# Optimization experiments

Measured on AMD Instinct MI355X. Metric: run time of the kernel, lower is better.

Reference implementation:

```python
import jax, jax.numpy as jnp
import numpy as np

N_NODES = 50000
N_EDGES = 800000
D = 128  # hidden_dim == node feature dim


def setup_inputs() -> dict:
    key = jax.random.key(0)
    k1, k2, k3, k4 = jax.random.split(key, 4)
    node_feat = jax.random.normal(k1, (N_NODES, D), dtype=jnp.float32)
    edge_index = jax.random.randint(k2, (2, N_EDGES), 0, N_NODES, dtype=jnp.int32)
    # MLP params: LazyLinear(2D -> D), Linear(D -> D)
    W1 = jax.random.normal(k3, (2 * D, D), dtype=jnp.float32) * (1.0 / np.sqrt(2 * D))
    b1 = jnp.zeros((D,), dtype=jnp.float32)
    W2 = jax.random.normal(k4, (D, D), dtype=jnp.float32) * (1.0 / np.sqrt(D))
    b2 = jnp.zeros((D,), dtype=jnp.float32)
    return {"node_feat": node_feat, "edge_index": edge_index,
            "W1": W1, "b1": b1, "W2": W2, "b2": b2}


def reference(node_feat, edge_index, W1, b1, W2, b2):
    # node_feat: [N, D]; edge_index: [2, E]
    src, dst = edge_index[0], edge_index[1]
    n = node_feat.shape[0]
    # gather source feats [E, D], scatter-add into dst -> [N, D]
    msgs = node_feat[src]
    agg = jax.ops.segment_sum(msgs, dst, num_segments=n)
    # degree normalization (clamp min 1)
    deg = jax.ops.segment_sum(jnp.ones_like(dst, dtype=node_feat.dtype), dst,
                              num_segments=n)
    agg = agg / jnp.maximum(deg, 1.0)[:, None]
    # update MLP on concat([node_feat, agg]); dropout is identity at eval
    h = jnp.concatenate([node_feat, agg], axis=-1)          # [N, 2D]
    h = jax.nn.relu(h @ W1 + b1)                             # [N, D]
    h = jax.nn.relu(h @ W2 + b2)                             # [N, D]
    return h
```

## Files before the change

kernel.cpp:

```cpp
#include <hip/hip_runtime.h>
#include <hip/hip_bf16.h>

#define N_NODES 50000
#define N_EDGES 800000
#define D 128
#define SLOTS 64
#define NTILES 782

typedef __attribute__((ext_vector_type(8))) short short8v;
typedef __attribute__((ext_vector_type(4))) float f32x4;


__device__ __forceinline__ unsigned short f32_to_bf16_rn(float f) {
    unsigned int u = __float_as_uint(f);
    unsigned int r = (u + 0x7fffu + ((u >> 16) & 1u)) >> 16;
    return (unsigned short)r;
}
__device__ __forceinline__ unsigned int pack2(float a, float b) {
    return (unsigned int)f32_to_bf16_rn(a) |
           ((unsigned int)f32_to_bf16_rn(b) << 16);
}
__device__ __forceinline__ float bflo(unsigned int w) {
    return __uint_as_float(w << 16);
}
__device__ __forceinline__ float bfhi(unsigned int w) {
    return __uint_as_float(w & 0xffff0000u);
}

__global__ __launch_bounds__(256) void fill_kernel(
    const int* __restrict__ ei, const float* __restrict__ W1,
    const float* __restrict__ W2, int* __restrict__ cnt,
    unsigned short* __restrict__ ss, unsigned short* __restrict__ Wt1,
    unsigned short* __restrict__ Wt2) {
    int tid = blockIdx.x * 256 + threadIdx.x;
    if (tid < N_EDGES) {
        int dst = ei[N_EDGES + tid];
        int pos = atomicAdd(&cnt[dst], 1);
        if (pos < SLOTS)
            ss[(size_t)dst * SLOTS + pos] = (unsigned short)ei[tid];
    }
    int t2 = tid - N_EDGES;
    if (t2 >= 0 && t2 < 128 * 256) {
        int n = t2 >> 8, k = t2 & 255;
        Wt1[t2] = f32_to_bf16_rn(W1[k * 128 + n]);
    }
    int t3 = t2 - 128 * 256;
    if (t3 >= 0 && t3 < 128 * 128) {
        int n = t3 >> 7, k = t3 & 127;
        Wt2[t3] = f32_to_bf16_rn(W2[k * 128 + n]);
    }
}

__global__ __launch_bounds__(256) void prep_kernel(
    const float* __restrict__ x, unsigned short* __restrict__ xb) {
    const int XBW = N_NODES * D / 8;
    int tid = blockIdx.x * 256 + threadIdx.x;
    if (tid >= XBW) return;
    const float4* p = reinterpret_cast<const float4*>(x + (size_t)tid * 8);
    float4 v0 = p[0], v1 = p[1];
    uint4 o;
    o.x = pack2(v0.x, v0.y);
    o.y = pack2(v0.z, v0.w);
    o.z = pack2(v1.x, v1.y);
    o.w = pack2(v1.z, v1.w);
    *reinterpret_cast<uint4*>(xb + (size_t)tid * 8) = o;
}

__global__ __launch_bounds__(256) void aggregate_kernel(
    const unsigned short* __restrict__ xb, const int* __restrict__ cnt,
    const unsigned short* __restrict__ ss, unsigned short* __restrict__ ab) {
    const int lane = threadIdx.x & 63;
    const int row = blockIdx.x * 4 + (threadIdx.x >> 6);
    int dg = cnt[row];
    if (dg > SLOTS) dg = SLOTS;
    const unsigned short* sp = ss + (size_t)row * SLOTS;
    float fx = 0.0f, fy = 0.0f;
    int j = 0;
    for (; j + 4 <= dg; j += 4) {
        int s0 = sp[j + 0];
        int s1 = sp[j + 1];
        int s2 = sp[j + 2];
        int s3 = sp[j + 3];
        unsigned int g0 = reinterpret_cast<const unsigned int*>(xb + (size_t)s0 * D)[lane];
        unsigned int g1 = reinterpret_cast<const unsigned int*>(xb + (size_t)s1 * D)[lane];
        unsigned int g2 = reinterpret_cast<const unsigned int*>(xb + (size_t)s2 * D)[lane];
        unsigned int g3 = reinterpret_cast<const unsigned int*>(xb + (size_t)s3 * D)[lane];
        fx += bflo(g0) + bflo(g1) + bflo(g2) + bflo(g3);
        fy += bfhi(g0) + bfhi(g1) + bfhi(g2) + bfhi(g3);
    }
    for (; j < dg; ++j) {
        int s0 = sp[j];
        unsigned int g0 = reinterpret_cast<const unsigned int*>(xb + (size_t)s0 * D)[lane];
        fx += bflo(g0);
        fy += bfhi(g0);
    }
    const float inv = 1.0f / fmaxf((float)dg, 1.0f);
    reinterpret_cast<unsigned int*>(ab + (size_t)row * D)[lane] =
        pack2(fx * inv, fy * inv);
}

__global__ __launch_bounds__(256, 1) void mlp_kernel(
    const unsigned short* __restrict__ xb, const unsigned short* __restrict__ ab,
    const unsigned short* __restrict__ Wt1,
    const unsigned short* __restrict__ Wt2, const float* __restrict__ b1,
    const float* __restrict__ b2, float* __restrict__ out) {
    __shared__ unsigned char w1s[65536];
    __shared__ unsigned char w2s[32768];
    __shared__ unsigned char h1t[4][4096];

    const int tid = threadIdx.x;
    for (int i = tid; i < 4096; i += 256) {
        unsigned o = (unsigned)i * 16;
        uint4 v = reinterpret_cast<const uint4*>(Wt1)[i];
        *reinterpret_cast<uint4*>(w1s + (o ^ (((o >> 9) & 7u) << 4))) = v;
    }
    for (int i = tid; i < 2048; i += 256) {
        unsigned o = (unsigned)i * 16;
        uint4 v = reinterpret_cast<const uint4*>(Wt2)[i];
        *reinterpret_cast<uint4*>(w2s + (o ^ (((o >> 8) & 7u) << 4))) = v;
    }

    const int lane = tid & 63;
    const int wv = tid >> 6;
    const int rloc = lane & 15;
    const int kseg = lane >> 4;
    const unsigned rswz = (unsigned)((rloc & 7) << 4);
    unsigned char* my = h1t[wv];

    float bias1[8], bias2[8];
#pragma unroll
    for (int ct = 0; ct < 8; ++ct) {
        bias1[ct] = b1[ct * 16 + rloc];
        bias2[ct] = b2[ct * 16 + rloc];
    }
    __syncthreads();

    for (int tile = blockIdx.x; tile < NTILES; tile += gridDim.x) {
        const int rbase = tile * 64 + wv * 16;
        int arow = rbase + rloc;
        if (arow >= N_NODES) arow = N_NODES - 1;

        short8v a[8];
#pragma unroll
        for (int kk = 0; kk < 8; ++kk) {
            const unsigned short* ap =
                (kk < 4) ? xb + (size_t)arow * D + kk * 32 + kseg * 8
                         : ab + (size_t)arow * D + (kk - 4) * 32 + kseg * 8;
            a[kk] = *reinterpret_cast<const short8v*>(ap);
        }
        f32x4 acc[8];
#pragma unroll
        for (int ct = 0; ct < 8; ++ct) acc[ct] = (f32x4){0.f, 0.f, 0.f, 0.f};
#pragma unroll
        for (int kk = 0; kk < 8; ++kk) {
#pragma unroll
            for (int ct = 0; ct < 8; ++ct) {
                unsigned off = (unsigned)((ct * 16 + rloc) * 512 + kk * 64 + kseg * 16);
                short8v b = *reinterpret_cast<const short8v*>(w1s + (off ^ rswz));
                acc[ct] = __builtin_amdgcn_mfma_f32_16x16x32_bf16(a[kk], b, acc[ct], 0, 0, 0);
            }
        }
#pragma unroll
        for (int ct = 0; ct < 8; ++ct) {
#pragma unroll
            for (int r = 0; r < 4; ++r) {
                int lrow = kseg * 4 + r;
                float v = fmaxf(acc[ct][r] + bias1[ct], 0.0f);
                unsigned off = (unsigned)(lrow * 256 + (ct * 16 + rloc) * 2);
                *reinterpret_cast<unsigned short*>(
                    my + (off ^ ((unsigned)((lrow & 7) << 4)))) = f32_to_bf16_rn(v);
            }
        }
        __syncthreads();

        short8v a2[4];
#pragma unroll
        for (int kk = 0; kk < 4; ++kk) {
            unsigned off = (unsigned)(rloc * 256 + kk * 64 + kseg * 16);
            a2[kk] = *reinterpret_cast<const short8v*>(my + (off ^ rswz));
        }
        f32x4 acc2[8];
#pragma unroll
        for (int ct = 0; ct < 8; ++ct) acc2[ct] = (f32x4){0.f, 0.f, 0.f, 0.f};
#pragma unroll
        for (int kk = 0; kk < 4; ++kk) {
#pragma unroll
            for (int ct = 0; ct < 8; ++ct) {
                unsigned off = (unsigned)((ct * 16 + rloc) * 256 + kk * 64 + kseg * 16);
                short8v b = *reinterpret_cast<const short8v*>(w2s + (off ^ rswz));
                acc2[ct] = __builtin_amdgcn_mfma_f32_16x16x32_bf16(a2[kk], b, acc2[ct], 0, 0, 0);
            }
        }
        const int orow0 = rbase + kseg * 4;
#pragma unroll
        for (int ct = 0; ct < 8; ++ct) {
#pragma unroll
            for (int r = 0; r < 4; ++r) {
                int row = orow0 + r;
                if (row < N_NODES) {
                    out[(size_t)row * 128 + ct * 16 + rloc] =
                        fmaxf(acc2[ct][r] + bias2[ct], 0.0f);
                }
            }
        }
        __syncthreads();
    }
}

extern "C" void kernel_launch(void* const* d_in, const int* in_sizes, int n_in,
                              void* d_out, int out_size, void* d_ws,
                              size_t ws_size, hipStream_t stream) {
    const float* node_feat = (const float*)d_in[0];
    const int* ei = (const int*)d_in[1];
    const float* W1 = (const float*)d_in[2];
    const float* b1 = (const float*)d_in[3];
    const float* W2 = (const float*)d_in[4];
    const float* b2 = (const float*)d_in[5];
    float* out = (float*)d_out;

    int* cnt = (int*)d_ws;
    unsigned short* ss = (unsigned short*)(cnt + N_NODES);
    unsigned short* xb = ss + (size_t)N_NODES * SLOTS;
    unsigned short* ab = xb + (size_t)N_NODES * D;
    unsigned short* Wt1 = ab + (size_t)N_NODES * D;
    unsigned short* Wt2 = Wt1 + 128 * 256;

    const int fill_threads = N_EDGES + 128 * 256 + 128 * 128;

    hipMemsetAsync(cnt, 0, N_NODES * sizeof(int), stream);
    fill_kernel<<<(fill_threads + 255) / 256, 256, 0, stream>>>(
        ei, W1, W2, cnt, ss, Wt1, Wt2);
    prep_kernel<<<(N_NODES * D / 8 + 255) / 256, 256, 0, stream>>>(node_feat, xb);
    aggregate_kernel<<<N_NODES / 4, 256, 0, stream>>>(xb, cnt, ss, ab);
    mlp_kernel<<<256, 256, 0, stream>>>(xb, ab, Wt1, Wt2, b1, b2, out);
}
```

Baseline: 126.5 us.

## Bucket edges by destination range before slot fill to localize atomics

```diff
diff --git a/kernel.cpp b/kernel.cpp
--- a/kernel.cpp
+++ b/kernel.cpp
@@ -6,6 +6,9 @@
 #define D 128
 #define SLOTS 64
 #define NTILES 782
+#define NBKT 8
+#define BKT_ROWS 6250
+#define STREAM_CAP 16384
 
 typedef __attribute__((ext_vector_type(8))) short short8v;
 typedef __attribute__((ext_vector_type(4))) float f32x4;
@@ -27,19 +30,78 @@
     return __uint_as_float(w & 0xffff0000u);
 }
 
-__global__ __launch_bounds__(256) void fill_kernel(
-    const int* __restrict__ ei, const float* __restrict__ W1,
-    const float* __restrict__ W2, int* __restrict__ cnt,
-    unsigned short* __restrict__ ss, unsigned short* __restrict__ Wt1,
-    unsigned short* __restrict__ Wt2) {
+__global__ __launch_bounds__(256) void bucket_kernel(
+    const int* __restrict__ ei, int* __restrict__ scnt,
+    unsigned int* __restrict__ pairs) {
+    const int tid = blockIdx.x * 256 + threadIdx.x;
+    const int lane = threadIdx.x & 63;
+    const int g = blockIdx.x & 7;
+    int bkt = -1;
+    unsigned int pk = 0;
+    if (tid < N_EDGES) {
+        int src = ei[tid];
+        int dst = ei[N_EDGES + tid];
+        bkt = dst / BKT_ROWS;
+        pk = ((unsigned int)(dst - bkt * BKT_ROWS) << 16) | (unsigned int)src;
+    }
+#pragma unroll
+    for (int b = 0; b < NBKT; ++b) {
+        unsigned long long m = __ballot(bkt == b);
+        if (bkt == b) {
+            int leader = __ffsll((unsigned long long)m) - 1;
+            int cb = __popcll(m);
+            int base = 0;
+            if (lane == leader) base = atomicAdd(&scnt[(b * 8 + g) * 32], cb);
+            base = __shfl(base, leader);
+            int pos = base + __popcll(m & ((1ULL << lane) - 1ULL));
+            if (pos < STREAM_CAP)
+                pairs[(size_t)(b * 8 + g) * STREAM_CAP + pos] = pk;
+        }
+    }
+}
+
+__global__ __launch_bounds__(256) void scatter_kernel(
+    const unsigned int* __restrict__ pairs, const int* __restrict__ scnt,
+    int* __restrict__ cnt, unsigned short* __restrict__ ss) {
+    const int b = blockIdx.x & 7;
+    const int sub = blockIdx.x >> 3;
+    const int g = sub & 7;
+    const int chunk = sub >> 3;
+    const int sid = b * 8 + g;
+    int count = scnt[sid * 32];
+    if (count > STREAM_CAP) count = STREAM_CAP;
+    const int per = (count + 7) / 8;
+    const int lo = chunk * per;
+    int hi = lo + per;
+    if (hi > count) hi = count;
+    const unsigned int* sp = pairs + (size_t)sid * STREAM_CAP;
+    const int rowbase = b * BKT_ROWS;
+    for (int i = lo + threadIdx.x; i < hi; i += 256) {
+        unsigned int p = sp[i];
+        int dst = rowbase + (int)(p >> 16);
+        int src = (int)(p & 0xffffu);
+        int pos = atomicAdd(&cnt[dst], 1);
+        if (pos < SLOTS) ss[(size_t)dst * SLOTS + pos] = (unsigned short)src;
+    }
+}
+
+__global__ __launch_bounds__(256) void prep_kernel(
+    const float* __restrict__ x, const float* __restrict__ W1,
+    const float* __restrict__ W2, unsigned short* __restrict__ xb,
+    unsigned short* __restrict__ Wt1, unsigned short* __restrict__ Wt2) {
+    const int XBW = N_NODES * D / 8;
     int tid = blockIdx.x * 256 + threadIdx.x;
-    if (tid < N_EDGES) {
-        int dst = ei[N_EDGES + tid];
-        int pos = atomicAdd(&cnt[dst], 1);
-        if (pos < SLOTS)
-            ss[(size_t)dst * SLOTS + pos] = (unsigned short)ei[tid];
-    }
-    int t2 = tid - N_EDGES;
+    if (tid < XBW) {
+        const float4* p = reinterpret_cast<const float4*>(x + (size_t)tid * 8);
+        float4 v0 = p[0], v1 = p[1];
+        uint4 o;
+        o.x = pack2(v0.x, v0.y);
+        o.y = pack2(v0.z, v0.w);
+        o.z = pack2(v1.x, v1.y);
+        o.w = pack2(v1.z, v1.w);
+        *reinterpret_cast<uint4*>(xb + (size_t)tid * 8) = o;
+    }
+    int t2 = tid - XBW;
     if (t2 >= 0 && t2 < 128 * 256) {
         int n = t2 >> 8, k = t2 & 255;
         Wt1[t2] = f32_to_bf16_rn(W1[k * 128 + n]);
@@ -49,21 +111,6 @@
         int n = t3 >> 7, k = t3 & 127;
         Wt2[t3] = f32_to_bf16_rn(W2[k * 128 + n]);
     }
-}
-
-__global__ __launch_bounds__(256) void prep_kernel(
-    const float* __restrict__ x, unsigned short* __restrict__ xb) {
-    const int XBW = N_NODES * D / 8;
-    int tid = blockIdx.x * 256 + threadIdx.x;
-    if (tid >= XBW) return;
-    const float4* p = reinterpret_cast<const float4*>(x + (size_t)tid * 8);
-    float4 v0 = p[0], v1 = p[1];
-    uint4 o;
-    o.x = pack2(v0.x, v0.y);
-    o.y = pack2(v0.z, v0.w);
-    o.z = pack2(v1.x, v1.y);
-    o.w = pack2(v1.z, v1.w);
-    *reinterpret_cast<uint4*>(xb + (size_t)tid * 8) = o;
 }
 
 __global__ __launch_bounds__(256) void aggregate_kernel(
@@ -219,18 +266,22 @@
     float* out = (float*)d_out;
 
     int* cnt = (int*)d_ws;
-    unsigned short* ss = (unsigned short*)(cnt + N_NODES);
+    int* scnt = cnt + N_NODES;
+    unsigned int* pairs = (unsigned int*)(scnt + 64 * 32);
+    unsigned short* ss = (unsigned short*)(pairs + (size_t)64 * STREAM_CAP);
     unsigned short* xb = ss + (size_t)N_NODES * SLOTS;
     unsigned short* ab = xb + (size_t)N_NODES * D;
     unsigned short* Wt1 = ab + (size_t)N_NODES * D;
     unsigned short* Wt2 = Wt1 + 128 * 256;
 
-    const int fill_threads = N_EDGES + 128 * 256 + 128 * 128;
-
-    hipMemsetAsync(cnt, 0, N_NODES * sizeof(int), stream);
-    fill_kernel<<<(fill_threads + 255) / 256, 256, 0, stream>>>(
-        ei, W1, W2, cnt, ss, Wt1, Wt2);
-    prep_kernel<<<(N_NODES * D / 8 + 255) / 256, 256, 0, stream>>>(node_feat, xb);
+    const int XBW = N_NODES * D / 8;
+    const int prep_threads = XBW + 128 * 256 + 128 * 128;
+
+    hipMemsetAsync(cnt, 0, (N_NODES + 64 * 32) * sizeof(int), stream);
+    bucket_kernel<<<(N_EDGES + 255) / 256, 256, 0, stream>>>(ei, scnt, pairs);
+    scatter_kernel<<<512, 256, 0, stream>>>(pairs, scnt, cnt, ss);
+    prep_kernel<<<(prep_threads + 255) / 256, 256, 0, stream>>>(
+        node_feat, W1, W2, xb, Wt1, Wt2);
     aggregate_kernel<<<N_NODES / 4, 256, 0, stream>>>(xb, cnt, ss, ab);
     mlp_kernel<<<256, 256, 0, stream>>>(xb, ab, Wt1, Wt2, b1, b2, out);
 }
```

New measurement: 171.5 us. 1.36x slower.
